# Optimization experiments

Measured on AMD Instinct MI355X. Metric: run time of the kernel, lower is better.

## Reference

```python
import jax, jax.numpy as jnp
import numpy as np

B, L, C, H = 8, 1024, 1024, 16  # batch, seq_len, n_embed, n_head


def setup_inputs() -> dict:
    key = jax.random.key(0)
    k0, k1, k2 = jax.random.split(key, 3)
    s = 0.02  # init scale
    return {
        "x": jax.random.normal(k0, (B, L, C), jnp.float32),
        "W_qkv": jax.random.normal(k1, (C, 3 * C), jnp.float32) * s,  # (in, out) layout
        "b_qkv": jnp.zeros((3 * C,), jnp.float32),
        "W_proj": jax.random.normal(k2, (C, C), jnp.float32) * s,
        "b_proj": jnp.zeros((C,), jnp.float32),
    }


def reference(x, W_qkv, b_qkv, W_proj, b_proj):
    Bb, Ll, Cc = x.shape
    d = Cc // H  # head dim
    qkv = x @ W_qkv + b_qkv                      # (B, L, 3C)
    q, k, v = jnp.split(qkv, 3, axis=2)
    q = q.reshape(Bb, Ll, H, d).transpose(0, 2, 1, 3)  # (B, H, L, d)
    k = k.reshape(Bb, Ll, H, d).transpose(0, 2, 1, 3)
    v = v.reshape(Bb, Ll, H, d).transpose(0, 2, 1, 3)
    scale = 1.0 / np.sqrt(d).astype(np.float32)
    attn = jnp.einsum("bhid,bhjd->bhij", q, k) * scale  # (B, H, Lq, Lk)
    causal = jnp.tril(jnp.ones((Ll, Ll), dtype=bool))    # (Lq, Lk)
    attn = jnp.where(causal[None, None, :, :], attn, -jnp.inf)
    # NOTE: source uses F.softmax(attn, dim=2) -> softmax over the QUERY axis.
    attn = jax.nn.softmax(attn, axis=2)
    y = jnp.einsum("bhij,bhjd->bhid", attn, v)           # (B, H, L, d)
    y = y.transpose(0, 2, 1, 3).reshape(Bb, Ll, Cc)      # (B, L, C)
    return y @ W_proj + b_proj
```

## Files before the change

kernel.cpp:

```cpp
#include <hip/hip_runtime.h>

typedef unsigned short u16;
typedef unsigned int   u32;
using bf16x8 = __attribute__((ext_vector_type(8))) short;
using f32x4  = __attribute__((ext_vector_type(4))) float;
using f32x16 = __attribute__((ext_vector_type(16))) float;
using u32x4  = __attribute__((ext_vector_type(4))) u32;

static constexpr int Bb = 8, Ll = 1024, Cc = 1024, Hh = 16, Dd = 64;
static constexpr int Mrows = Bb * Ll;
static constexpr int N3    = 3 * Cc;
static constexpr float QSCALE = 0.125f * 1.44269504088896f;

__device__ __forceinline__ u16 f2b(float f) {
    u32 u = __builtin_bit_cast(u32, f);
    u += 0x7FFFu + ((u >> 16) & 1u);
    return (u16)(u >> 16);
}
__device__ __forceinline__ float b2f(u16 u) {
    return __builtin_bit_cast(float, (u32)u << 16);
}
__device__ __forceinline__ u32 pack2bf(float a, float b) {
    return (u32)f2b(a) | ((u32)f2b(b) << 16);
}
__device__ __forceinline__ void gload16(const u16* g, u16* l) {
    __builtin_amdgcn_global_load_lds(
        (const __attribute__((address_space(1))) void*)g,
        (__attribute__((address_space(3))) void*)l, 16, 0, 0);
}

__global__ void k_f32_to_bf16(const float* __restrict__ in, u16* __restrict__ out, int n16) {
    int idx = blockIdx.x * blockDim.x + threadIdx.x;
    if (idx >= n16) return;
    #pragma unroll
    for (int h = 0; h < 2; ++h) {
        f32x4 v0 = *((const f32x4*)in + idx * 4 + h * 2);
        f32x4 v1 = *((const f32x4*)in + idx * 4 + h * 2 + 1);
        u32x4 o;
        o[0] = pack2bf(v0[0], v0[1]);
        o[1] = pack2bf(v0[2], v0[3]);
        o[2] = pack2bf(v1[0], v1[1]);
        o[3] = pack2bf(v1[2], v1[3]);
        *((u32x4*)out + idx * 2 + h) = o;
    }
}

__global__ void k_transpose_w(const float* __restrict__ Wqkv, u16* __restrict__ WqkvT,
                              const float* __restrict__ Wproj, u16* __restrict__ WprojT) {
    __shared__ float tile[32][33];
    int bx = blockIdx.x;
    const float* in; u16* out; int Cn;
    if (bx < 96) { in = Wqkv;  out = WqkvT;  Cn = N3; }
    else         { in = Wproj; out = WprojT; Cn = Cc; bx -= 96; }
    const int R = Cc;
    int tx = threadIdx.x, ty = threadIdx.y;
    int c = bx * 32 + tx;
    int rbase = blockIdx.y * 32;
    #pragma unroll
    for (int rr = 0; rr < 4; ++rr)
        tile[ty + rr * 8][tx] = in[(size_t)(rbase + ty + rr * 8) * Cn + c];
    __syncthreads();
    int ro = bx * 32 + ty;
    #pragma unroll
    for (int rr = 0; rr < 4; ++rr)
        out[(size_t)(ro + rr * 8) * R + rbase + tx] = f2b(tile[tx][ty + rr * 8]);
}

__global__ void k_transpose_scale_bf16(const u16* __restrict__ in, const float* __restrict__ zinv,
                                       u16* __restrict__ out, int R, int Cn) {
    __shared__ u16 tile[32][33];
    int bh = blockIdx.z;
    size_t base = (size_t)bh * R * Cn;
    int tx = threadIdx.x, ty = threadIdx.y;
    int c = blockIdx.x * 32 + tx;
    int rbase = blockIdx.y * 32;
    #pragma unroll
    for (int rr = 0; rr < 4; ++rr)
        tile[ty + rr * 8][tx] = in[base + (size_t)(rbase + ty + rr * 8) * Cn + c];
    __syncthreads();
    float zv = zinv[(size_t)bh * R + rbase + tx];
    int ro = blockIdx.x * 32 + ty;
    #pragma unroll
    for (int rr = 0; rr < 4; ++rr)
        out[base + (size_t)(ro + rr * 8) * R + rbase + tx] = f2b(b2f(tile[tx][ty + rr * 8]) * zv);
}

__global__ __launch_bounds__(256, 2)
void k_gemm_qkv32(const u16* __restrict__ A, const u16* __restrict__ Bt,
                  const float* __restrict__ bias,
                  u16* __restrict__ qo, u16* __restrict__ ko, u16* __restrict__ vo)
{
    const int K = Cc;
    const int NT = K / 64;
    __shared__ u16 As[2][128 * 64];
    __shared__ u16 Bs[2][128 * 64];
    const int tid = threadIdx.x;
    const int wid = tid >> 6, lane = tid & 63;
    const int l31 = lane & 31, lhi = lane >> 5, l7 = lane & 7;
    const int wr = wid >> 1, wc = wid & 1;
    const int nwg = gridDim.x * gridDim.y;
    const int flat = blockIdx.y * gridDim.x + blockIdx.x;
    const int swz = (flat & 7) * (nwg >> 3) + (flat >> 3);
    const int bx = swz % gridDim.x, by = swz / gridDim.x;
    const int row0 = by * 128, col0 = bx * 128;

    const int srow = tid >> 3;
    const int schunk = (tid & 7) ^ (srow & 7);
    const u16* gA = A  + (size_t)(row0 + srow) * K + schunk * 8;
    const u16* gB = Bt + (size_t)(col0 + srow) * K + schunk * 8;

#define STG(buf, t) do { \
    const u16* ga_ = gA + (size_t)(t) * 64; \
    const u16* gb_ = gB + (size_t)(t) * 64; \
    u16* la_ = &As[buf][wid * 512]; \
    u16* lb_ = &Bs[buf][wid * 512]; \
    gload16(ga_,                  la_); \
    gload16(ga_ + (size_t)32 * K, la_ + 2048); \
    gload16(ga_ + (size_t)64 * K, la_ + 4096); \
    gload16(ga_ + (size_t)96 * K, la_ + 6144); \
    gload16(gb_,                  lb_); \
    gload16(gb_ + (size_t)32 * K, lb_ + 2048); \
    gload16(gb_ + (size_t)64 * K, lb_ + 4096); \
    gload16(gb_ + (size_t)96 * K, lb_ + 6144); \
} while (0)

    const int coff0 = (((0 + lhi) ^ l7) << 3);
    const int coff1 = (((2 + lhi) ^ l7) << 3);
    const int coff2 = (((4 + lhi) ^ l7) << 3);
    const int coff3 = (((6 + lhi) ^ l7) << 3);
    const int coff[4] = { coff0, coff1, coff2, coff3 };

    f32x16 acc[2][2] = {};

    STG(0, 0);
    STG(1, 1);
    asm volatile("s_waitcnt vmcnt(8)" ::: "memory");
    __builtin_amdgcn_s_barrier();
    __builtin_amdgcn_sched_barrier(0);

    for (int t = 0; t < NT; ++t) {
        const u16* cA = &As[t & 1][0];
        const u16* cB = &Bs[t & 1][0];
        bf16x8 af[2][4], bf0[4];
        #pragma unroll
        for (int tm = 0; tm < 2; ++tm)
            #pragma unroll
            for (int kc = 0; kc < 4; ++kc)
                af[tm][kc] = *(const bf16x8*)&cA[(wr * 64 + tm * 32 + l31) * 64 + coff[kc]];
        #pragma unroll
        for (int kc = 0; kc < 4; ++kc)
            bf0[kc] = *(const bf16x8*)&cB[(wc * 64 + l31) * 64 + coff[kc]];
        __builtin_amdgcn_s_setprio(1);
        #pragma unroll
        for (int tm = 0; tm < 2; ++tm)
            #pragma unroll
            for (int kc = 0; kc < 4; ++kc)
                acc[tm][0] = __builtin_amdgcn_mfma_f32_32x32x16_bf16(
                    af[tm][kc], bf0[kc], acc[tm][0], 0, 0, 0);
        __builtin_amdgcn_s_setprio(0);
        __builtin_amdgcn_s_barrier();
        bf16x8 bf1[4];
        #pragma unroll
        for (int kc = 0; kc < 4; ++kc)
            bf1[kc] = *(const bf16x8*)&cB[(wc * 64 + 32 + l31) * 64 + coff[kc]];
        __builtin_amdgcn_s_setprio(1);
        #pragma unroll
        for (int tm = 0; tm < 2; ++tm)
            #pragma unroll
            for (int kc = 0; kc < 4; ++kc)
                acc[tm][1] = __builtin_amdgcn_mfma_f32_32x32x16_bf16(
                    af[tm][kc], bf1[kc], acc[tm][1], 0, 0, 0);
        __builtin_amdgcn_s_setprio(0);
        __builtin_amdgcn_s_barrier();
        __builtin_amdgcn_sched_barrier(0);
        if (t + 2 < NT) STG(t & 1, t + 2);
        if (t + 1 < NT) {
            if (t + 2 < NT) { asm volatile("s_waitcnt vmcnt(8)" ::: "memory"); }
            else            { asm volatile("s_waitcnt vmcnt(0)" ::: "memory"); }
            __builtin_amdgcn_s_barrier();
            __builtin_amdgcn_sched_barrier(0);
        }
    }
#undef STG

    #pragma unroll
    for (int tm = 0; tm < 2; ++tm) {
        #pragma unroll
        for (int tn = 0; tn < 2; ++tn) {
            int cg = col0 + wc * 64 + tn * 32 + l31;
            float bv = bias[cg];
            int which = cg >> 10;
            float sc = (which == 0) ? QSCALE : 1.0f;
            int cc2 = cg & 1023;
            int h = cc2 >> 6, dd = cc2 & 63;
            int rbase = row0 + wr * 64 + tm * 32 + 4 * lhi;
            #pragma unroll
            for (int g = 0; g < 4; ++g) {
                #pragma unroll
                for (int r = 0; r < 4; ++r) {
                    int rg = rbase + 8 * g + r;
                    int bidx = rg >> 10, ll2 = rg & 1023;
                    size_t o = ((size_t)(bidx * Hh + h) * Ll + ll2) * Dd + dd;
                    u16 val = f2b((acc[tm][tn][g * 4 + r] + bv) * sc);
                    if (which == 0) qo[o] = val;
                    else if (which == 1) ko[o] = val;
                    else vo[o] = val;
                }
            }
        }
    }
}

__global__ __launch_bounds__(256)
void k_gemm_proj(const u16* __restrict__ A, const u16* __restrict__ Bt,
                 const float* __restrict__ bias, float* __restrict__ outf)
{
    const int N = Cc, K = Cc;
    __shared__ u16 As[2][128 * 32];
    __shared__ u16 Bs[2][128 * 32];
    const int tid = threadIdx.x;
    const int wid = tid >> 6, lane = tid & 63;
    const int lr = lane & 15, lg = lane >> 4;
    const int wr = wid >> 1, wc = wid & 1;
    const int nwg = gridDim.x * gridDim.y;
    const int flat = blockIdx.y * gridDim.x + blockIdx.x;
    const int swz = (flat & 7) * (nwg >> 3) + (flat >> 3);
    const int bx = swz % gridDim.x, by = swz / gridDim.x;
    const int row0 = by * 128, col0 = bx * 128;

    const int srow = wid * 32 + (lane >> 2);
    const int schk = (lane & 3) ^ (srow & 3);
    const u16* aP = A  + (size_t)(row0 + srow) * K + schk * 8;
    const u16* bP = Bt + (size_t)(col0 + srow) * K + schk * 8;
    const size_t r16 = (size_t)16 * K;
    u16* aL0 = &As[0][wid * 32 * 32]; u16* aL0b = aL0 + 16 * 32;
    u16* bL0 = &Bs[0][wid * 32 * 32]; u16* bL0b = bL0 + 16 * 32;
    u16* aL1 = &As[1][wid * 32 * 32]; u16* aL1b = aL1 + 16 * 32;
    u16* bL1 = &Bs[1][wid * 32 * 32]; u16* bL1b = bL1 + 16 * 32;

    f32x4 acc[4][4] = {};

#define STAGE0(kk) { gload16(aP + (kk), aL0); gload16(aP + r16 + (kk), aL0b); \
                     gload16(bP + (kk), bL0); gload16(bP + r16 + (kk), bL0b); }
#define STAGE1(kk) { gload16(aP + (kk), aL1); gload16(aP + r16 + (kk), aL1b); \
                     gload16(bP + (kk), bL1); gload16(bP + r16 + (kk), bL1b); }
#define COMPUTE(bufi) { \
        bf16x8 af[4], bfv[4]; \
        _Pragma("unroll") \
        for (int m = 0; m < 4; ++m) { int rw = wr * 64 + m * 16 + lr; \
            af[m] = *(const bf16x8*)&As[bufi][rw * 32 + ((lg ^ (rw & 3)) * 8)]; } \
        _Pragma("unroll") \
        for (int n = 0; n < 4; ++n) { int rw = wc * 64 + n * 16 + lr; \
            bfv[n] = *(const bf16x8*)&Bs[bufi][rw * 32 + ((lg ^ (rw & 3)) * 8)]; } \
        _Pragma("unroll") \
        for (int m = 0; m < 4; ++m) \
            _Pragma("unroll") \
            for (int n = 0; n < 4; ++n) \
                acc[m][n] = __builtin_amdgcn_mfma_f32_16x16x32_bf16(af[m], bfv[n], acc[m][n], 0, 0, 0); }

    STAGE0(0);
    __syncthreads();
    for (int k0 = 0; k0 < K; k0 += 64) {
        if (k0 + 32 < K) STAGE1(k0 + 32);
        COMPUTE(0);
        __syncthreads();
        if (k0 + 64 < K) STAGE0(k0 + 64);
        COMPUTE(1);
        __syncthreads();
    }
#undef STAGE0
#undef STAGE1
#undef COMPUTE

    #pragma unroll
    for (int m = 0; m < 4; ++m) {
        int rb2 = row0 + wr * 64 + m * 16 + lg * 4;
        #pragma unroll
        for (int n = 0; n < 4; ++n) {
            int cg = col0 + wc * 64 + n * 16 + lr;
            float bv = bias[cg];
            #pragma unroll
            for (int r = 0; r < 4; ++r)
                outf[(size_t)(rb2 + r) * N + cg] = acc[m][n][r] + bv;
        }
    }
}

__global__ __launch_bounds__(256)
void k_attn_colsum(const u16* __restrict__ Q, const u16* __restrict__ Kb,
                   float* __restrict__ zinv)
{
    const int tid = threadIdx.x;
    const int wid = tid >> 6, lane = tid & 63;
    const int lr = lane & 15, lg = lane >> 4;
    const int fid = blockIdx.x;
    const int xcd = fid & 7, n = fid >> 3;
    const int pr = n & 3;
    const int bh = (xcd << 4) | (n >> 2);
    const u16* Qp = Q  + (size_t)bh * Ll * Dd;
    const u16* Kp = Kb + (size_t)bh * Ll * Dd;
    const bool dmask[4] = { lg * 4 + 0 >= lr, lg * 4 + 1 >= lr,
                            lg * 4 + 2 >= lr, lg * 4 + 3 >= lr };

    #pragma unroll
    for (int t = 0; t < 2; ++t) {
        const int xt = t ? (7 - pr) : pr;
        const int jw = xt * 128 + wid * 32;
        bf16x8 kb[2][2];
        #pragma unroll
        for (int g = 0; g < 2; ++g) {
            kb[g][0] = *(const bf16x8*)&Kp[(jw + g * 16 + lr) * Dd + lg * 8];
            kb[g][1] = *(const bf16x8*)&Kp[(jw + g * 16 + lr) * Dd + 32 + lg * 8];
        }
        float z0 = 0.f, z1 = 0.f;
        {
            bf16x8 qa0 = *(const bf16x8*)&Qp[(jw + lr) * Dd + lg * 8];
            bf16x8 qa1 = *(const bf16x8*)&Qp[(jw + lr) * Dd + 32 + lg * 8];
            f32x4 s = {0.f, 0.f, 0.f, 0.f};
            s = __builtin_amdgcn_mfma_f32_16x16x32_bf16(qa0, kb[0][0], s, 0, 0, 0);
            s = __builtin_amdgcn_mfma_f32_16x16x32_bf16(qa1, kb[0][1], s, 0, 0, 0);
            #pragma unroll
            for (int r = 0; r < 4; ++r) z0 += dmask[r] ? exp2f(s[r]) : 0.f;
        }
        {
            bf16x8 qa0 = *(const bf16x8*)&Qp[(jw + 16 + lr) * Dd + lg * 8];
            bf16x8 qa1 = *(const bf16x8*)&Qp[(jw + 16 + lr) * Dd + 32 + lg * 8];
            f32x4 s0 = {0.f, 0.f, 0.f, 0.f}, s1 = {0.f, 0.f, 0.f, 0.f};
            s0 = __builtin_amdgcn_mfma_f32_16x16x32_bf16(qa0, kb[0][0], s0, 0, 0, 0);
            s0 = __builtin_amdgcn_mfma_f32_16x16x32_bf16(qa1, kb[0][1], s0, 0, 0, 0);
            s1 = __builtin_amdgcn_mfma_f32_16x16x32_bf16(qa0, kb[1][0], s1, 0, 0, 0);
            s1 = __builtin_amdgcn_mfma_f32_16x16x32_bf16(qa1, kb[1][1], s1, 0, 0, 0);
            #pragma unroll
            for (int r = 0; r < 4; ++r) {
                z0 += exp2f(s0[r]);
                z1 += dmask[r] ? exp2f(s1[r]) : 0.f;
            }
        }
        for (int ib = jw + 32; ib < Ll; ib += 16) {
            bf16x8 qa0 = *(const bf16x8*)&Qp[(ib + lr) * Dd + lg * 8];
            bf16x8 qa1 = *(const bf16x8*)&Qp[(ib + lr) * Dd + 32 + lg * 8];
            f32x4 s0 = {0.f, 0.f, 0.f, 0.f}, s1 = {0.f, 0.f, 0.f, 0.f};
            s0 = __builtin_amdgcn_mfma_f32_16x16x32_bf16(qa0, kb[0][0], s0, 0, 0, 0);
            s0 = __builtin_amdgcn_mfma_f32_16x16x32_bf16(qa1, kb[0][1], s0, 0, 0, 0);
            s1 = __builtin_amdgcn_mfma_f32_16x16x32_bf16(qa0, kb[1][0], s1, 0, 0, 0);
            s1 = __builtin_amdgcn_mfma_f32_16x16x32_bf16(qa1, kb[1][1], s1, 0, 0, 0);
            #pragma unroll
            for (int r = 0; r < 4; ++r) { z0 += exp2f(s0[r]); z1 += exp2f(s1[r]); }
        }
        z0 += __shfl_xor(z0, 16); z0 += __shfl_xor(z0, 32);
        z1 += __shfl_xor(z1, 16); z1 += __shfl_xor(z1, 32);
        if (lg == 0) {
            zinv[(size_t)bh * Ll + jw + lr]      = 1.f / z0;
            zinv[(size_t)bh * Ll + jw + 16 + lr] = 1.f / z1;
        }
    }
}

__global__ __launch_bounds__(256, 4)
void k_attn_pv(const u16* __restrict__ Q, const u16* __restrict__ Kb,
               const u16* __restrict__ Vt, u16* __restrict__ Y)
{
    __shared__ u16 Ks[2][64 * 64];
    __shared__ u16 Vs[2][64 * 64];
    const int tid = threadIdx.x;
    const int wid = tid >> 6, lane = tid & 63;
    const int lr = lane & 15, lg = lane >> 4;
    const int l7 = lr & 7;
    const int fid = blockIdx.x;
    const int xcd = fid & 7, n = fid >> 3;
    const int xtA = n & 7;
    const int xtB = 15 - xtA;
    const int bh = (xcd << 4) | (n >> 3);
    const int bidx = bh >> 4, h = bh & 15;
    const u16* Qp = Q  + (size_t)bh * Ll * Dd;
    const u16* Kp = Kb + (size_t)bh * Ll * Dd;
    const u16* Vp = Vt + (size_t)bh * Ll * Dd;
    const int src0 = lr + 32 * (lg & 1);
    const int src1 = src0 + 16;
    const bool selHi = (lg & 2) != 0;
    const int ch0 = ((lg ^ l7) << 3);
    const int ch1 = (((4 + lg) ^ l7) << 3);
    const int srow = tid >> 3;
    const int schunk = (tid & 7) ^ (srow & 7);

    const int iwA = xtA * 64 + wid * 16;
    const int iwB = xtB * 64 + wid * 16;
    bf16x8 qaA0 = *(const bf16x8*)&Qp[(iwA + lr) * Dd + lg * 8];
    bf16x8 qaA1 = *(const bf16x8*)&Qp[(iwA + lr) * Dd + 32 + lg * 8];
    bf16x8 qaB0 = *(const bf16x8*)&Qp[(iwB + lr) * Dd + lg * 8];
    bf16x8 qaB1 = *(const bf16x8*)&Qp[(iwB + lr) * Dd + 32 + lg * 8];
    f32x4 yaccA[4] = {};
    f32x4 yaccB[4] = {};

    const int NS = 17;
#define JOF(s) (((s) <= xtA) ? 64 * (s) : 64 * ((s) - xtA - 1))

#define STGKV(buf, J) do { \
    const u16* gk_ = Kp + (size_t)((J) + srow) * 64 + schunk * 8; \
    const u16* gv_ = Vp + (size_t)srow * Ll + (J) + schunk * 8; \
    u16* lk_ = &Ks[buf][wid * 512]; \
    u16* lv_ = &Vs[buf][wid * 512]; \
    gload16(gk_,                   lk_); \
    gload16(gk_ + (size_t)32 * 64, lk_ + 2048); \
    gload16(gv_,                   lv_); \
    gload16(gv_ + (size_t)32 * Ll, lv_ + 2048); \
} while (0)

#define PV_STEP(buf, J0, IW, QA0, QA1, YACC) do { \
    const u16* Ks_ = &Ks[buf][0]; \
    const u16* Vs_ = &Vs[buf][0]; \
    uint2 w0, w1, w2, w3; \
    _Pragma("unroll") \
    for (int cs = 0; cs < 4; ++cs) { \
        bf16x8 kb0 = *(const bf16x8*)&Ks_[(cs * 16 + lr) * 64 + ch0]; \
        bf16x8 kb1 = *(const bf16x8*)&Ks_[(cs * 16 + lr) * 64 + ch1]; \
        f32x4 s_ = {0.f, 0.f, 0.f, 0.f}; \
        s_ = __builtin_amdgcn_mfma_f32_16x16x32_bf16(kb0, QA0, s_, 0, 0, 0); \
        s_ = __builtin_amdgcn_mfma_f32_16x16x32_bf16(kb1, QA1, s_, 0, 0, 0); \
        int jb = (J0) + cs * 16; \
        float p[4]; \
        if (jb + 15 <= (IW)) { \
            _Pragma("unroll") \
            for (int r = 0; r < 4; ++r) p[r] = exp2f(s_[r]); \
        } else { \
            int ig = (IW) + lr; \
            _Pragma("unroll") \
            for (int r = 0; r < 4; ++r) \
                p[r] = (jb + 4 * lg + r <= ig) ? exp2f(s_[r]) : 0.f; \
        } \
        uint2 w_; \
        w_.x = pack2bf(p[0], p[1]); \
        w_.y = pack2bf(p[2], p[3]); \
        if (cs == 0) w0 = w_; else if (cs == 1) w1 = w_; \
        else if (cs == 2) w2 = w_; else w3 = w_; \
    } \
    u32 a00 = (u32)__shfl((int)w0.x, src0), a01 = (u32)__shfl((int)w0.y, src0); \
    u32 a02 = (u32)__shfl((int)w0.x, src1), a03 = (u32)__shfl((int)w0.y, src1); \
    u32 a10 = (u32)__shfl((int)w1.x, src0), a11 = (u32)__shfl((int)w1.y, src0); \
    u32 a12 = (u32)__shfl((int)w1.x, src1), a13 = (u32)__shfl((int)w1.y, src1); \
    u32 a20 = (u32)__shfl((int)w2.x, src0), a21 = (u32)__shfl((int)w2.y, src0); \
    u32 a22 = (u32)__shfl((int)w2.x, src1), a23 = (u32)__shfl((int)w2.y, src1); \
    u32 a30 = (u32)__shfl((int)w3.x, src0), a31 = (u32)__shfl((int)w3.y, src0); \
    u32 a32 = (u32)__shfl((int)w3.x, src1), a33 = (u32)__shfl((int)w3.y, src1); \
    u32x4 pa0u, pa1u; \
    pa0u[0] = selHi ? a10 : a00;  pa0u[1] = selHi ? a11 : a01; \
    pa0u[2] = selHi ? a12 : a02;  pa0u[3] = selHi ? a13 : a03; \
    pa1u[0] = selHi ? a30 : a20;  pa1u[1] = selHi ? a31 : a21; \
    pa1u[2] = selHi ? a32 : a22;  pa1u[3] = selHi ? a33 : a23; \
    bf16x8 pa0 = __builtin_bit_cast(bf16x8, pa0u); \
    bf16x8 pa1 = __builtin_bit_cast(bf16x8, pa1u); \
    _Pragma("unroll") \
    for (int ns = 0; ns < 4; ++ns) { \
        bf16x8 vb0 = *(const bf16x8*)&Vs_[(ns * 16 + lr) * 64 + ch0]; \
        bf16x8 vb1 = *(const bf16x8*)&Vs_[(ns * 16 + lr) * 64 + ch1]; \
        YACC[ns] = __builtin_amdgcn_mfma_f32_16x16x32_bf16(pa0, vb0, YACC[ns], 0, 0, 0); \
        YACC[ns] = __builtin_amdgcn_mfma_f32_16x16x32_bf16(pa1, vb1, YACC[ns], 0, 0, 0); \
    } \
} while (0)

    STGKV(0, 0);
    STGKV(1, JOF(1));
    asm volatile("s_waitcnt vmcnt(4)" ::: "memory");
    __builtin_amdgcn_s_barrier();
    __builtin_amdgcn_sched_barrier(0);

    for (int s = 0; s < NS; ++s) {
        if (s <= xtA) { PV_STEP((s & 1), 64 * s, iwA, qaA0, qaA1, yaccA); }
        else          { PV_STEP((s & 1), 64 * (s - xtA - 1), iwB, qaB0, qaB1, yaccB); }
        __builtin_amdgcn_s_barrier();
        __builtin_amdgcn_sched_barrier(0);
        if (s + 2 < NS) STGKV((s & 1), JOF(s + 2));
        if (s + 1 < NS) {
            if (s + 2 < NS) { asm volatile("s_waitcnt vmcnt(4)" ::: "memory"); }
            else            { asm volatile("s_waitcnt vmcnt(0)" ::: "memory"); }
            __builtin_amdgcn_s_barrier();
            __builtin_amdgcn_sched_barrier(0);
        }
    }
#undef STGKV
#undef PV_STEP
#undef JOF

    #pragma unroll
    for (int ns = 0; ns < 4; ++ns)
        #pragma unroll
        for (int r = 0; r < 4; ++r) {
            int l2 = iwA + lg * 4 + r;
            Y[((size_t)bidx * Ll + l2) * Cc + h * Dd + ns * 16 + lr] = f2b(yaccA[ns][r]);
        }
    #pragma unroll
    for (int ns = 0; ns < 4; ++ns)
        #pragma unroll
        for (int r = 0; r < 4; ++r) {
            int l2 = iwB + lg * 4 + r;
            Y[((size_t)bidx * Ll + l2) * Cc + h * Dd + ns * 16 + lr] = f2b(yaccB[ns][r]);
        }
}

extern "C" void kernel_launch(void* const* d_in, const int* in_sizes, int n_in,
                              void* d_out, int out_size, void* d_ws, size_t ws_size,
                              hipStream_t stream)
{
    const float* x     = (const float*)d_in[0];
    const float* Wqkv  = (const float*)d_in[1];
    const float* bqkv  = (const float*)d_in[2];
    const float* Wproj = (const float*)d_in[3];
    const float* bproj = (const float*)d_in[4];
    float* out = (float*)d_out;

    char* ws = (char*)d_ws;
    u16* xb     = (u16*)(ws + 0);
    u16* WqkvT  = (u16*)(ws + 16777216);
    u16* WprojT = (u16*)(ws + 23068672);
    u16* q      = (u16*)(ws + 25165824);
    u16* k      = (u16*)(ws + 41943040);
    u16* v      = (u16*)(ws + 58720256);
    u16* vt     = (u16*)(ws + 75497472);
    float* zinv = (float*)(ws + 92274688);

    k_f32_to_bf16<<<dim3(2048), dim3(256), 0, stream>>>(x, xb, Mrows * Cc / 16);
    k_transpose_w<<<dim3(128, 32), dim3(32, 8), 0, stream>>>(Wqkv, WqkvT, Wproj, WprojT);
    k_gemm_qkv32<<<dim3(N3 / 128, Mrows / 128), dim3(256), 0, stream>>>(
        xb, WqkvT, bqkv, q, k, v);
    k_attn_colsum<<<dim3(512), dim3(256), 0, stream>>>(q, k, zinv);
    k_transpose_scale_bf16<<<dim3(2, 32, Bb * Hh), dim3(32, 8), 0, stream>>>(v, zinv, vt, Ll, Dd);
    k_attn_pv<<<dim3(1024), dim3(256), 0, stream>>>(q, k, vt, v);
    k_gemm_proj<<<dim3(Cc / 128, Mrows / 128), dim3(256), 0, stream>>>(
        v, WprojT, bproj, out);
}
```

Baseline: 198.3 us.

## Stage Q tiles through shared memory in column-sum kernel with paired tiles

```diff
diff --git a/kernel.cpp b/kernel.cpp
--- a/kernel.cpp
+++ b/kernel.cpp
@@ -286,73 +286,97 @@
     }
 }
 
-__global__ __launch_bounds__(256)
+__global__ __launch_bounds__(256, 4)
 void k_attn_colsum(const u16* __restrict__ Q, const u16* __restrict__ Kb,
                    float* __restrict__ zinv)
 {
+    __shared__ u16 Qs[2][64 * 64];
     const int tid = threadIdx.x;
     const int wid = tid >> 6, lane = tid & 63;
     const int lr = lane & 15, lg = lane >> 4;
+    const int l7 = lr & 7;
     const int fid = blockIdx.x;
     const int xcd = fid & 7, n = fid >> 3;
-    const int pr = n & 3;
-    const int bh = (xcd << 4) | (n >> 2);
+    const int xtA = n & 7;
+    const int xtB = 15 - xtA;
+    const int bh = (xcd << 4) | (n >> 3);
     const u16* Qp = Q  + (size_t)bh * Ll * Dd;
     const u16* Kp = Kb + (size_t)bh * Ll * Dd;
+    const int jwA = xtA * 64 + wid * 16;
+    const int jwB = xtB * 64 + wid * 16;
+    bf16x8 kbA0 = *(const bf16x8*)&Kp[(jwA + lr) * Dd + lg * 8];
+    bf16x8 kbA1 = *(const bf16x8*)&Kp[(jwA + lr) * Dd + 32 + lg * 8];
+    bf16x8 kbB0 = *(const bf16x8*)&Kp[(jwB + lr) * Dd + lg * 8];
+    bf16x8 kbB1 = *(const bf16x8*)&Kp[(jwB + lr) * Dd + 32 + lg * 8];
     const bool dmask[4] = { lg * 4 + 0 >= lr, lg * 4 + 1 >= lr,
                             lg * 4 + 2 >= lr, lg * 4 + 3 >= lr };
-
-    #pragma unroll
-    for (int t = 0; t < 2; ++t) {
-        const int xt = t ? (7 - pr) : pr;
-        const int jw = xt * 128 + wid * 32;
-        bf16x8 kb[2][2];
-        #pragma unroll
-        for (int g = 0; g < 2; ++g) {
-            kb[g][0] = *(const bf16x8*)&Kp[(jw + g * 16 + lr) * Dd + lg * 8];
-            kb[g][1] = *(const bf16x8*)&Kp[(jw + g * 16 + lr) * Dd + 32 + lg * 8];
-        }
-        float z0 = 0.f, z1 = 0.f;
-        {
-            bf16x8 qa0 = *(const bf16x8*)&Qp[(jw + lr) * Dd + lg * 8];
-            bf16x8 qa1 = *(const bf16x8*)&Qp[(jw + lr) * Dd + 32 + lg * 8];
-            f32x4 s = {0.f, 0.f, 0.f, 0.f};
-            s = __builtin_amdgcn_mfma_f32_16x16x32_bf16(qa0, kb[0][0], s, 0, 0, 0);
-            s = __builtin_amdgcn_mfma_f32_16x16x32_bf16(qa1, kb[0][1], s, 0, 0, 0);
-            #pragma unroll
-            for (int r = 0; r < 4; ++r) z0 += dmask[r] ? exp2f(s[r]) : 0.f;
-        }
-        {
-            bf16x8 qa0 = *(const bf16x8*)&Qp[(jw + 16 + lr) * Dd + lg * 8];
-            bf16x8 qa1 = *(const bf16x8*)&Qp[(jw + 16 + lr) * Dd + 32 + lg * 8];
-            f32x4 s0 = {0.f, 0.f, 0.f, 0.f}, s1 = {0.f, 0.f, 0.f, 0.f};
-            s0 = __builtin_amdgcn_mfma_f32_16x16x32_bf16(qa0, kb[0][0], s0, 0, 0, 0);
-            s0 = __builtin_amdgcn_mfma_f32_16x16x32_bf16(qa1, kb[0][1], s0, 0, 0, 0);
-            s1 = __builtin_amdgcn_mfma_f32_16x16x32_bf16(qa0, kb[1][0], s1, 0, 0, 0);
-            s1 = __builtin_amdgcn_mfma_f32_16x16x32_bf16(qa1, kb[1][1], s1, 0, 0, 0);
-            #pragma unroll
-            for (int r = 0; r < 4; ++r) {
-                z0 += exp2f(s0[r]);
-                z1 += dmask[r] ? exp2f(s1[r]) : 0.f;
-            }
-        }
-        for (int ib = jw + 32; ib < Ll; ib += 16) {
-            bf16x8 qa0 = *(const bf16x8*)&Qp[(ib + lr) * Dd + lg * 8];
-            bf16x8 qa1 = *(const bf16x8*)&Qp[(ib + lr) * Dd + 32 + lg * 8];
-            f32x4 s0 = {0.f, 0.f, 0.f, 0.f}, s1 = {0.f, 0.f, 0.f, 0.f};
-            s0 = __builtin_amdgcn_mfma_f32_16x16x32_bf16(qa0, kb[0][0], s0, 0, 0, 0);
-            s0 = __builtin_amdgcn_mfma_f32_16x16x32_bf16(qa1, kb[0][1], s0, 0, 0, 0);
-            s1 = __builtin_amdgcn_mfma_f32_16x16x32_bf16(qa0, kb[1][0], s1, 0, 0, 0);
-            s1 = __builtin_amdgcn_mfma_f32_16x16x32_bf16(qa1, kb[1][1], s1, 0, 0, 0);
-            #pragma unroll
-            for (int r = 0; r < 4; ++r) { z0 += exp2f(s0[r]); z1 += exp2f(s1[r]); }
-        }
-        z0 += __shfl_xor(z0, 16); z0 += __shfl_xor(z0, 32);
-        z1 += __shfl_xor(z1, 16); z1 += __shfl_xor(z1, 32);
-        if (lg == 0) {
-            zinv[(size_t)bh * Ll + jw + lr]      = 1.f / z0;
-            zinv[(size_t)bh * Ll + jw + 16 + lr] = 1.f / z1;
-        }
+    const int ch0 = ((lg ^ l7) << 3);
+    const int ch1 = (((4 + lg) ^ l7) << 3);
+    const int srow = tid >> 3;
+    const int schunk = (tid & 7) ^ (srow & 7);
+    float zA = 0.f, zB = 0.f;
+
+    const int nA = 16 - xtA;
+    const int NS = 17;
+#define IOF(s) (((s) < nA) ? (xtA * 64 + 64 * (s)) : (xtB * 64 + 64 * ((s) - nA)))
+
+#define STGQ(buf, I0) do { \
+    const u16* g_ = Qp + (size_t)((I0) + srow) * 64 + schunk * 8; \
+    u16* l_ = &Qs[buf][wid * 512]; \
+    gload16(g_,                   l_); \
+    gload16(g_ + (size_t)32 * 64, l_ + 2048); \
+} while (0)
+
+#define CS_STEP(buf, I0, JW, KB0, KB1, ZACC) do { \
+    const u16* Qs_ = &Qs[buf][0]; \
+    _Pragma("unroll") \
+    for (int ss = 0; ss < 4; ++ss) { \
+        int ib = (I0) + ss * 16; \
+        if (ib >= (JW)) { \
+            bf16x8 qa0 = *(const bf16x8*)&Qs_[(ss * 16 + lr) * 64 + ch0]; \
+            bf16x8 qa1 = *(const bf16x8*)&Qs_[(ss * 16 + lr) * 64 + ch1]; \
+            f32x4 s_ = {0.f, 0.f, 0.f, 0.f}; \
+            s_ = __builtin_amdgcn_mfma_f32_16x16x32_bf16(qa0, KB0, s_, 0, 0, 0); \
+            s_ = __builtin_amdgcn_mfma_f32_16x16x32_bf16(qa1, KB1, s_, 0, 0, 0); \
+            if (ib >= (JW) + 16) { \
+                _Pragma("unroll") \
+                for (int r = 0; r < 4; ++r) ZACC += exp2f(s_[r]); \
+            } else { \
+                _Pragma("unroll") \
+                for (int r = 0; r < 4; ++r) ZACC += dmask[r] ? exp2f(s_[r]) : 0.f; \
+            } \
+        } \
+    } \
+} while (0)
+
+    STGQ(0, IOF(0));
+    STGQ(1, IOF(1));
+    asm volatile("s_waitcnt vmcnt(2)" ::: "memory");
+    __builtin_amdgcn_s_barrier();
+    __builtin_amdgcn_sched_barrier(0);
+
+    for (int s = 0; s < NS; ++s) {
+        if (s < nA) { CS_STEP((s & 1), xtA * 64 + 64 * s, jwA, kbA0, kbA1, zA); }
+        else        { CS_STEP((s & 1), xtB * 64 + 64 * (s - nA), jwB, kbB0, kbB1, zB); }
+        __builtin_amdgcn_s_barrier();
+        __builtin_amdgcn_sched_barrier(0);
+        if (s + 2 < NS) STGQ((s & 1), IOF(s + 2));
+        if (s + 1 < NS) {
+            if (s + 2 < NS) { asm volatile("s_waitcnt vmcnt(2)" ::: "memory"); }
+            else            { asm volatile("s_waitcnt vmcnt(0)" ::: "memory"); }
+            __builtin_amdgcn_s_barrier();
+            __builtin_amdgcn_sched_barrier(0);
+        }
+    }
+#undef STGQ
+#undef CS_STEP
+#undef IOF
+
+    zA += __shfl_xor(zA, 16); zA += __shfl_xor(zA, 32);
+    zB += __shfl_xor(zB, 16); zB += __shfl_xor(zB, 32);
+    if (lg == 0) {
+        zinv[(size_t)bh * Ll + jwA + lr] = 1.f / zA;
+        zinv[(size_t)bh * Ll + jwB + lr] = 1.f / zB;
     }
 }
 
@@ -522,7 +546,7 @@
     k_transpose_w<<<dim3(128, 32), dim3(32, 8), 0, stream>>>(Wqkv, WqkvT, Wproj, WprojT);
     k_gemm_qkv32<<<dim3(N3 / 128, Mrows / 128), dim3(256), 0, stream>>>(
         xb, WqkvT, bqkv, q, k, v);
-    k_attn_colsum<<<dim3(512), dim3(256), 0, stream>>>(q, k, zinv);
+    k_attn_colsum<<<dim3(1024), dim3(256), 0, stream>>>(q, k, zinv);
     k_transpose_scale_bf16<<<dim3(2, 32, Bb * Hh), dim3(32, 8), 0, stream>>>(v, zinv, vt, Ll, Dd);
     k_attn_pv<<<dim3(1024), dim3(256), 0, stream>>>(q, k, vt, v);
     k_gemm_proj<<<dim3(Cc / 128, Mrows / 128), dim3(256), 0, stream>>>(
```

New measurement: 188.8 us. 1.05x faster.
